# Optimization experiments

Measured on AMD Instinct MI355X. Metric: run time of the kernel, lower is better.

## Reference

```python
import jax, jax.numpy as jnp
import numpy as np

D_MODEL, D_K, D_V = 1024, 64, 64
B, S = 4, 4096


def setup_inputs() -> dict:
    key = jax.random.key(0)
    ks = jax.random.split(key, 13)
    s = 1.0 / np.sqrt(D_MODEL)
    inp = {
        "q": jax.random.normal(ks[0], (B, S, D_MODEL), jnp.float32),
        "k": jax.random.normal(ks[1], (B, S, D_MODEL), jnp.float32),
        "v": jax.random.normal(ks[2], (B, S, D_MODEL), jnp.float32),
        "mask": jax.random.randint(ks[3], (1, S, S), 0, 2, jnp.int32),
        "Wq": jax.random.normal(ks[4], (D_K, D_MODEL), jnp.float32) * s,
        "bq": jax.random.normal(ks[5], (D_K,), jnp.float32) * s,
        "Wk": jax.random.normal(ks[6], (D_K, D_MODEL), jnp.float32) * s,
        "bk": jax.random.normal(ks[7], (D_K,), jnp.float32) * s,
        "Wv": jax.random.normal(ks[8], (D_V, D_MODEL), jnp.float32) * s,
        "bv": jax.random.normal(ks[9], (D_V,), jnp.float32) * s,
        "Wo": jax.random.normal(ks[10], (D_MODEL, D_V), jnp.float32) / np.sqrt(D_V),
        "bo": jax.random.normal(ks[11], (D_MODEL,), jnp.float32) / np.sqrt(D_V),
    }
    return inp


def reference(q, k, v, mask, Wq, bq, Wk, bk, Wv, bv, Wo, bo):
    # linear projections (torch Linear: x @ W.T + b)
    qh = jnp.einsum("bsd,kd->bsk", q, Wq) + bq   # [B,S,d_k]
    kh = jnp.einsum("bsd,kd->bsk", k, Wk) + bk   # [B,S,d_k]
    vh = jnp.einsum("bsd,vd->bsv", v, Wv) + bv   # [B,S,d_v]
    scale = 1.0 / jnp.sqrt(jnp.float32(D_K))
    scores = jnp.einsum("bqk,bmk->bqm", qh, kh) * scale  # [B,S,S]
    scores = jnp.where(mask == 0, jnp.float32(-1e9), scores)
    attn = jax.nn.softmax(scores, axis=-1)
    out = jnp.einsum("bqm,bmv->bqv", attn, vh)   # [B,S,d_v]
    return jnp.einsum("bqv,dv->bqd", out, Wo) + bo
```

## Files before the change

kernel.cpp:

```cpp
#include <hip/hip_runtime.h>
#include <cmath>

typedef __attribute__((ext_vector_type(8))) short bf16x8;
typedef __attribute__((ext_vector_type(4))) short bf16x4;
typedef __attribute__((ext_vector_type(4))) float f32x4;

constexpr int B_ = 4;
constexpr int S_ = 4096;
constexpr int DM_ = 1024;
constexpr int DK_ = 64;
constexpr int NROW = B_ * S_;

__device__ __forceinline__ short f2bf(float x) {
  union { float f; unsigned u; } c; c.f = x;
  unsigned r = (c.u + 0x7FFF + ((c.u >> 16) & 1)) >> 16;
  return (short)r;
}
__device__ __forceinline__ float bf2f(short h) {
  union { float f; unsigned u; } c; c.u = ((unsigned)(unsigned short)h) << 16;
  return c.f;
}

__global__ __launch_bounds__(256) void maskpack(
    const int* __restrict__ mask, unsigned long long* __restrict__ bits) {
  const int wid = (blockIdx.x * 256 + threadIdx.x) >> 6;
  const int lane = threadIdx.x & 63;
  const size_t base = (size_t)wid * 4096;
  for (int it = 0; it < 64; ++it) {
    int m = mask[base + it * 64 + lane];
    unsigned long long b = __ballot(m != 0);
    if (lane == 0) bits[(size_t)wid * 64 + it] = b;
  }
}

__global__ __launch_bounds__(256) void proj_mfma(
    const float* __restrict__ q, const float* __restrict__ k,
    const float* __restrict__ v,
    const float* __restrict__ Wq, const float* __restrict__ bq,
    const float* __restrict__ Wk, const float* __restrict__ bk,
    const float* __restrict__ Wv, const float* __restrict__ bv,
    short* __restrict__ qh, short* __restrict__ kh, short* __restrict__ vhT) {
  const int mat = blockIdx.z;
  const float* X    = mat == 0 ? q  : (mat == 1 ? k  : v);
  const float* W    = mat == 0 ? Wq : (mat == 1 ? Wk : Wv);
  const float* bias = mat == 0 ? bq : (mat == 1 ? bk : bv);

  __shared__ float Xs[128][68];
  __shared__ short Ws[64][72];

  const int t = threadIdx.x;
  const int row0 = blockIdx.x * 128;
  const int lane = t & 63, w = t >> 6, quad = lane >> 4, l16 = lane & 15;

  f32x4 acc[2][4] = {};

  for (int k0 = 0; k0 < DM_; k0 += 64) {
    __syncthreads();
    {
      const int rr = t >> 3, cc = (t & 7) * 8;
#pragma unroll
      for (int pass = 0; pass < 4; ++pass) {
        int r = pass * 32 + rr;
        const float* src = X + (size_t)(row0 + r) * DM_ + k0 + cc;
        *(f32x4*)&Xs[r][cc]     = *(const f32x4*)src;
        *(f32x4*)&Xs[r][cc + 4] = *(const f32x4*)(src + 4);
      }
    }
    {
      int c = t >> 2, kk = (t & 3) * 16;
      const float* src = W + (size_t)c * DM_ + k0 + kk;
      f32x4 a0 = *(const f32x4*)src, a1 = *(const f32x4*)(src + 4);
      f32x4 a2 = *(const f32x4*)(src + 8), a3 = *(const f32x4*)(src + 12);
      bf16x8 w0, w1;
#pragma unroll
      for (int j = 0; j < 4; ++j) {
        w0[j] = f2bf(a0[j]); w0[j + 4] = f2bf(a1[j]);
        w1[j] = f2bf(a2[j]); w1[j + 4] = f2bf(a3[j]);
      }
      *(bf16x8*)&Ws[c][kk]     = w0;
      *(bf16x8*)&Ws[c][kk + 8] = w1;
    }
    __syncthreads();

#pragma unroll
    for (int c = 0; c < 2; ++c) {
      bf16x8 bw[4];
#pragma unroll
      for (int ct = 0; ct < 4; ++ct)
        bw[ct] = *(const bf16x8*)&Ws[16 * ct + l16][c * 32 + quad * 8];
#pragma unroll
      for (int rt = 0; rt < 2; ++rt) {
        const float* xp = &Xs[32 * w + 16 * rt + l16][c * 32 + quad * 8];
        f32x4 x0 = *(const f32x4*)xp;
        f32x4 x1 = *(const f32x4*)(xp + 4);
        bf16x8 ahi, alo;
#pragma unroll
        for (int j = 0; j < 4; ++j) {
          short h0 = f2bf(x0[j]); ahi[j] = h0;     alo[j]     = f2bf(x0[j] - bf2f(h0));
          short h1 = f2bf(x1[j]); ahi[j + 4] = h1; alo[j + 4] = f2bf(x1[j] - bf2f(h1));
        }
#pragma unroll
        for (int ct = 0; ct < 4; ++ct) {
          acc[rt][ct] = __builtin_amdgcn_mfma_f32_16x16x32_bf16(ahi, bw[ct], acc[rt][ct], 0, 0, 0);
          acc[rt][ct] = __builtin_amdgcn_mfma_f32_16x16x32_bf16(alo, bw[ct], acc[rt][ct], 0, 0, 0);
        }
      }
    }
  }

  float bs[4];
#pragma unroll
  for (int ct = 0; ct < 4; ++ct) bs[ct] = bias[16 * ct + l16];

  short* dstq = (mat == 0) ? qh : kh;
#pragma unroll
  for (int rt = 0; rt < 2; ++rt)
#pragma unroll
    for (int ct = 0; ct < 4; ++ct)
#pragma unroll
      for (int reg = 0; reg < 4; ++reg) {
        int r = row0 + 32 * w + 16 * rt + quad * 4 + reg;
        int c = 16 * ct + l16;
        short hv = f2bf(acc[rt][ct][reg] + bs[ct]);
        if (mat == 2)
          vhT[((size_t)(r >> 12) * DK_ + c) * S_ + (r & 4095)] = hv;
        else
          dstq[(size_t)r * DK_ + c] = hv;
      }
}

__global__ __launch_bounds__(256) void attn_mfma(
    const short* __restrict__ qh, const short* __restrict__ kh,
    const short* __restrict__ vhT, const unsigned int* __restrict__ mbits,
    float* __restrict__ Opart, float* __restrict__ mpart,
    float* __restrict__ lpart, int ns) {
  __shared__ short ks[64][72];
  __shared__ short vt[64][72];
  __shared__ short ps[4][16][72];

  const int b = blockIdx.z;
  const int split = blockIdx.y;
  const int q0 = blockIdx.x * 64;
  const int t = threadIdx.x, lane = t & 63, w = t >> 6;
  const int quad = lane >> 4, l16 = lane & 15;
  const int myq = q0 + 16 * w + l16;

  const int kt0 = split * (S_ / ns);
  const int kt1 = kt0 + S_ / ns;

  bf16x8 qf[2];
  {
    const short* src = qh + ((size_t)b * S_ + myq) * DK_ + quad * 8;
    qf[0] = *(const bf16x8*)src;
    qf[1] = *(const bf16x8*)(src + 32);
  }

  f32x4 ao[4] = {};
  float m_i = -INFINITY, l_i = 0.0f;

  const int sr = t >> 2;
  const int sseg = t & 3;

  for (int kt = kt0; kt < kt1; kt += 64) {
    __syncthreads();
    {
      const short* srck = kh + ((size_t)b * S_ + kt + sr) * DK_;
      *(bf16x8*)&ks[sr][8 * sseg]       = *(const bf16x8*)(srck + 8 * sseg);
      *(bf16x8*)&ks[sr][8 * (sseg + 4)] = *(const bf16x8*)(srck + 8 * (sseg + 4));
      const short* srcv = vhT + ((size_t)b * DK_ + sr) * S_ + kt;
      *(bf16x8*)&vt[sr][8 * sseg]       = *(const bf16x8*)(srcv + 8 * sseg);
      *(bf16x8*)&vt[sr][8 * (sseg + 4)] = *(const bf16x8*)(srcv + 8 * (sseg + 4));
    }
    const uint2 mw = *(const uint2*)&mbits[(size_t)myq * 128 + (kt >> 5)];
    __syncthreads();

    f32x4 sacc[4] = {};
#pragma unroll
    for (int c = 0; c < 2; ++c)
#pragma unroll
      for (int tt = 0; tt < 4; ++tt) {
        bf16x8 a = *(const bf16x8*)&ks[16 * tt + l16][c * 32 + quad * 8];
        sacc[tt] = __builtin_amdgcn_mfma_f32_16x16x32_bf16(a, qf[c], sacc[tt], 0, 0, 0);
      }

    float sc[16];
#pragma unroll
    for (int tt = 0; tt < 4; ++tt) {
      unsigned wrd = (tt & 2) ? mw.y : mw.x;
      int base = (tt & 1) * 16 + quad * 4;
#pragma unroll
      for (int r = 0; r < 4; ++r)
        sc[tt * 4 + r] = ((wrd >> (base + r)) & 1) ? sacc[tt][r] * 0.125f : -1e9f;
    }

    float mx = sc[0];
#pragma unroll
    for (int i = 1; i < 16; ++i) mx = fmaxf(mx, sc[i]);
    mx = fmaxf(mx, __shfl_xor(mx, 16));
    mx = fmaxf(mx, __shfl_xor(mx, 32));
    float m_new = fmaxf(m_i, mx);
    float alpha = __expf(m_i - m_new);
    float p[16], sum = 0.0f;
#pragma unroll
    for (int i = 0; i < 16; ++i) { p[i] = __expf(sc[i] - m_new); sum += p[i]; }
    sum += __shfl_xor(sum, 16);
    sum += __shfl_xor(sum, 32);
    l_i = l_i * alpha + sum;
    m_i = m_new;

#pragma unroll
    for (int tt = 0; tt < 4; ++tt) {
      bf16x4 pk;
#pragma unroll
      for (int r = 0; r < 4; ++r) pk[r] = f2bf(p[tt * 4 + r]);
      *(bf16x4*)&ps[w][l16][16 * tt + quad * 4] = pk;
    }

#pragma unroll
    for (int dt = 0; dt < 4; ++dt)
#pragma unroll
      for (int r = 0; r < 4; ++r) ao[dt][r] *= alpha;

#pragma unroll
    for (int c = 0; c < 2; ++c) {
      bf16x8 bp = *(const bf16x8*)&ps[w][l16][c * 32 + quad * 8];
#pragma unroll
      for (int dt = 0; dt < 4; ++dt) {
        bf16x8 av = *(const bf16x8*)&vt[16 * dt + l16][c * 32 + quad * 8];
        ao[dt] = __builtin_amdgcn_mfma_f32_16x16x32_bf16(av, bp, ao[dt], 0, 0, 0);
      }
    }
  }

  const size_t prow = (size_t)split * NROW + (size_t)b * S_ + myq;
#pragma unroll
  for (int dt = 0; dt < 4; ++dt)
    *(f32x4*)&Opart[prow * DK_ + 16 * dt + quad * 4] = ao[dt];
  if (quad == 0) {
    mpart[prow] = m_i;
    lpart[prow] = l_i;
  }
}

__global__ __launch_bounds__(256) void attn_combine(
    const float* __restrict__ Opart, const float* __restrict__ mpart,
    const float* __restrict__ lpart, short* __restrict__ o_bf, int ns) {
  const int t = threadIdx.x;
  const int row = blockIdx.x * 64 + (t >> 2);
  const int c0 = (t & 3) * 16;

  float M = -INFINITY;
  for (int s = 0; s < ns; ++s) M = fmaxf(M, mpart[(size_t)s * NROW + row]);
  float L = 0.0f, wt[4];
  for (int s = 0; s < ns; ++s) {
    wt[s] = __expf(mpart[(size_t)s * NROW + row] - M);
    L += wt[s] * lpart[(size_t)s * NROW + row];
  }
  float acc[16] = {};
  for (int s = 0; s < ns; ++s) {
    const float* src = Opart + ((size_t)s * NROW + row) * DK_ + c0;
#pragma unroll
    for (int j = 0; j < 16; j += 4) {
      f32x4 vv = *(const f32x4*)(src + j);
#pragma unroll
      for (int r = 0; r < 4; ++r) acc[j + r] += wt[s] * vv[r];
    }
  }
  const float inv = 1.0f / L;
  bf16x8 o0, o1;
#pragma unroll
  for (int j = 0; j < 8; ++j) {
    o0[j] = f2bf(acc[j] * inv);
    o1[j] = f2bf(acc[j + 8] * inv);
  }
  *(bf16x8*)&o_bf[(size_t)row * DK_ + c0]     = o0;
  *(bf16x8*)&o_bf[(size_t)row * DK_ + c0 + 8] = o1;
}

__global__ __launch_bounds__(256) void outproj_mfma(
    const short* __restrict__ o_bf, const float* __restrict__ Wo,
    const float* __restrict__ bo, float* __restrict__ out) {
  __shared__ short os[64][72];
  __shared__ short wos[256][72];

  const int t = threadIdx.x, lane = t & 63, w = t >> 6;
  const int quad = lane >> 4, l16 = lane & 15;
  const int s0 = blockIdx.y * 64;
  const int dm0 = blockIdx.x * 256;

  {
    int r = t >> 2, cq = (t & 3) * 16;
    const short* src = o_bf + (size_t)(s0 + r) * DK_ + cq;
    *(bf16x8*)&os[r][cq]     = *(const bf16x8*)src;
    *(bf16x8*)&os[r][cq + 8] = *(const bf16x8*)(src + 8);
  }
#pragma unroll
  for (int pass = 0; pass < 4; ++pass) {
    int r = pass * 64 + (t >> 2), cq = (t & 3) * 16;
    const float* src = Wo + (size_t)(dm0 + r) * DK_ + cq;
    f32x4 a0 = *(const f32x4*)src, a1 = *(const f32x4*)(src + 4);
    f32x4 a2 = *(const f32x4*)(src + 8), a3 = *(const f32x4*)(src + 12);
    bf16x8 v0, v1;
#pragma unroll
    for (int j = 0; j < 4; ++j) {
      v0[j] = f2bf(a0[j]); v0[j + 4] = f2bf(a1[j]);
      v1[j] = f2bf(a2[j]); v1[j + 4] = f2bf(a3[j]);
    }
    *(bf16x8*)&wos[r][cq]     = v0;
    *(bf16x8*)&wos[r][cq + 8] = v1;
  }
  __syncthreads();

  bf16x8 af[2];
#pragma unroll
  for (int c = 0; c < 2; ++c)
    af[c] = *(const bf16x8*)&os[16 * w + l16][c * 32 + quad * 8];

  f32x4 acc[16] = {};
#pragma unroll
  for (int c = 0; c < 2; ++c)
#pragma unroll
    for (int nt = 0; nt < 16; ++nt) {
      bf16x8 bw = *(const bf16x8*)&wos[16 * nt + l16][c * 32 + quad * 8];
      acc[nt] = __builtin_amdgcn_mfma_f32_16x16x32_bf16(af[c], bw, acc[nt], 0, 0, 0);
    }

  float bias_r[16];
#pragma unroll
  for (int nt = 0; nt < 16; ++nt) bias_r[nt] = bo[dm0 + 16 * nt + l16];

#pragma unroll
  for (int nt = 0; nt < 16; ++nt)
#pragma unroll
    for (int reg = 0; reg < 4; ++reg) {
      int s = s0 + 16 * w + quad * 4 + reg;
      int dm = dm0 + 16 * nt + l16;
      out[(size_t)s * DM_ + dm] = acc[nt][reg] + bias_r[nt];
    }
}

extern "C" void kernel_launch(void* const* d_in, const int* in_sizes, int n_in,
                              void* d_out, int out_size, void* d_ws,
                              size_t ws_size, hipStream_t stream) {
  (void)in_sizes; (void)n_in; (void)out_size;
  const float* q  = (const float*)d_in[0];
  const float* k  = (const float*)d_in[1];
  const float* v  = (const float*)d_in[2];
  const int* mask = (const int*)d_in[3];
  const float* Wq = (const float*)d_in[4];
  const float* bq = (const float*)d_in[5];
  const float* Wk = (const float*)d_in[6];
  const float* bk = (const float*)d_in[7];
  const float* Wv = (const float*)d_in[8];
  const float* bv = (const float*)d_in[9];
  const float* Wo = (const float*)d_in[10];
  const float* bo = (const float*)d_in[11];
  float* out = (float*)d_out;

  short* qh  = (short*)d_ws;
  short* kh  = qh + (size_t)NROW * DK_;
  short* vhT = kh + (size_t)NROW * DK_;
  unsigned int* mbits = (unsigned int*)(vhT + (size_t)NROW * DK_);
  short* o_bf = (short*)(mbits + (size_t)S_ * 128);
  float* mpart = (float*)(o_bf + (size_t)NROW * DK_);
  float* lpart = mpart + 4 * NROW;
  float* Opart = lpart + 4 * NROW;

  const size_t base_bytes = (size_t)((char*)Opart - (char*)d_ws);
  const size_t per_split = (size_t)NROW * DK_ * sizeof(float);
  int ns = 1;
  if (ws_size >= base_bytes + 4 * per_split) ns = 4;
  else if (ws_size >= base_bytes + 2 * per_split) ns = 2;

  maskpack<<<1024, 256, 0, stream>>>(mask, (unsigned long long*)mbits);
  proj_mfma<<<dim3(NROW / 128, 1, 3), 256, 0, stream>>>(
      q, k, v, Wq, bq, Wk, bk, Wv, bv, qh, kh, vhT);
  attn_mfma<<<dim3(S_ / 64, ns, B_), 256, 0, stream>>>(
      qh, kh, vhT, mbits, Opart, mpart, lpart, ns);
  attn_combine<<<NROW / 64, 256, 0, stream>>>(Opart, mpart, lpart, o_bf, ns);
  outproj_mfma<<<dim3(DM_ / 256, NROW / 64), 256, 0, stream>>>(o_bf, Wo, bo, out);
}
```

Measured before the change: 390.1 us.

## Double-buffer projection GEMM with async global-to-LDS loads and pre-converted bf16 weights

Folds the weight fp32→bf16 conversion into the mask-packing prep kernel, so the projection kernel reads bf16 weights directly. The projection GEMM now uses direct global_load_lds into XOR-swizzled, double-buffered LDS tiles, overlapping the next tile's load with MFMA compute. Rows per block drop from 128 to 64 to raise block count. The bf16 weights are stored in the Opart workspace region, which later attention kernels overwrite; this is safe only because of stream ordering.

Result: faster. 380.3 us (-2.5%).

```diff
diff --git a/kernel.cpp b/kernel.cpp
--- a/kernel.cpp
+++ b/kernel.cpp
@@ -4,6 +4,9 @@
 typedef __attribute__((ext_vector_type(8))) short bf16x8;
 typedef __attribute__((ext_vector_type(4))) short bf16x4;
 typedef __attribute__((ext_vector_type(4))) float f32x4;
+typedef unsigned int u32;
+typedef __attribute__((address_space(1))) const u32 gu32;
+typedef __attribute__((address_space(3))) u32 lu32;
 
 constexpr int B_ = 4;
 constexpr int S_ = 4096;
@@ -20,92 +23,120 @@
   union { float f; unsigned u; } c; c.u = ((unsigned)(unsigned short)h) << 16;
   return c.f;
 }
-
-__global__ __launch_bounds__(256) void maskpack(
-    const int* __restrict__ mask, unsigned long long* __restrict__ bits) {
-  const int wid = (blockIdx.x * 256 + threadIdx.x) >> 6;
-  const int lane = threadIdx.x & 63;
-  const size_t base = (size_t)wid * 4096;
-  for (int it = 0; it < 64; ++it) {
-    int m = mask[base + it * 64 + lane];
-    unsigned long long b = __ballot(m != 0);
-    if (lane == 0) bits[(size_t)wid * 64 + it] = b;
+__device__ __forceinline__ void gl16(const void* g, void* l) {
+  __builtin_amdgcn_global_load_lds((gu32*)g, (lu32*)l, 16, 0, 0);
+}
+
+__global__ __launch_bounds__(256) void prep(
+    const int* __restrict__ mask, unsigned long long* __restrict__ bits,
+    const float* __restrict__ Wq, const float* __restrict__ Wk,
+    const float* __restrict__ Wv, short* __restrict__ wbf) {
+  if (blockIdx.x < 1024) {
+    const int wid = (blockIdx.x * 256 + threadIdx.x) >> 6;
+    const int lane = threadIdx.x & 63;
+    const size_t base = (size_t)wid * 4096;
+    for (int it = 0; it < 64; ++it) {
+      int m = mask[base + it * 64 + lane];
+      unsigned long long b = __ballot(m != 0);
+      if (lane == 0) bits[(size_t)wid * 64 + it] = b;
+    }
+  } else {
+    const int mat = blockIdx.x - 1024;
+    const float* W = mat == 0 ? Wq : (mat == 1 ? Wk : Wv);
+    short* dst = wbf + (size_t)mat * DK_ * DM_;
+    const int t = threadIdx.x;
+#pragma unroll 4
+    for (int i = 0; i < 32; ++i) {
+      int idx = i * 2048 + t * 8;
+      f32x4 a0 = *(const f32x4*)(W + idx);
+      f32x4 a1 = *(const f32x4*)(W + idx + 4);
+      bf16x8 h;
+#pragma unroll
+      for (int j = 0; j < 4; ++j) { h[j] = f2bf(a0[j]); h[j + 4] = f2bf(a1[j]); }
+      *(bf16x8*)(dst + idx) = h;
+    }
   }
 }
 
 __global__ __launch_bounds__(256) void proj_mfma(
     const float* __restrict__ q, const float* __restrict__ k,
-    const float* __restrict__ v,
-    const float* __restrict__ Wq, const float* __restrict__ bq,
-    const float* __restrict__ Wk, const float* __restrict__ bk,
-    const float* __restrict__ Wv, const float* __restrict__ bv,
+    const float* __restrict__ v, const short* __restrict__ wbf,
+    const float* __restrict__ bq, const float* __restrict__ bk,
+    const float* __restrict__ bv,
     short* __restrict__ qh, short* __restrict__ kh, short* __restrict__ vhT) {
+  __shared__ __align__(16) char smem[49152];
+
   const int mat = blockIdx.z;
-  const float* X    = mat == 0 ? q  : (mat == 1 ? k  : v);
-  const float* W    = mat == 0 ? Wq : (mat == 1 ? Wk : Wv);
+  const char* Xb = (const char*)(mat == 0 ? q : (mat == 1 ? k : v));
+  const char* Wb = (const char*)(wbf + (size_t)mat * DK_ * DM_);
   const float* bias = mat == 0 ? bq : (mat == 1 ? bk : bv);
 
-  __shared__ float Xs[128][68];
-  __shared__ short Ws[64][72];
-
   const int t = threadIdx.x;
-  const int row0 = blockIdx.x * 128;
+  const int row0 = blockIdx.x * 64;
   const int lane = t & 63, w = t >> 6, quad = lane >> 4, l16 = lane & 15;
 
-  f32x4 acc[2][4] = {};
-
-  for (int k0 = 0; k0 < DM_; k0 += 64) {
-    __syncthreads();
-    {
-      const int rr = t >> 3, cc = (t & 7) * 8;
-#pragma unroll
-      for (int pass = 0; pass < 4; ++pass) {
-        int r = pass * 32 + rr;
-        const float* src = X + (size_t)(row0 + r) * DM_ + k0 + cc;
-        *(f32x4*)&Xs[r][cc]     = *(const f32x4*)src;
-        *(f32x4*)&Xs[r][cc + 4] = *(const f32x4*)(src + 4);
-      }
-    }
-    {
-      int c = t >> 2, kk = (t & 3) * 16;
-      const float* src = W + (size_t)c * DM_ + k0 + kk;
-      f32x4 a0 = *(const f32x4*)src, a1 = *(const f32x4*)(src + 4);
-      f32x4 a2 = *(const f32x4*)(src + 8), a3 = *(const f32x4*)(src + 12);
-      bf16x8 w0, w1;
-#pragma unroll
-      for (int j = 0; j < 4; ++j) {
-        w0[j] = f2bf(a0[j]); w0[j + 4] = f2bf(a1[j]);
-        w1[j] = f2bf(a2[j]); w1[j + 4] = f2bf(a3[j]);
-      }
-      *(bf16x8*)&Ws[c][kk]     = w0;
-      *(bf16x8*)&Ws[c][kk + 8] = w1;
-    }
-    __syncthreads();
-
+  f32x4 acc[4] = {};
+
+  auto stage = [&](int buf, int ks) {
+    const int k0 = ks * 64;
+#pragma unroll
+    for (int i = 0; i < 4; ++i) {
+      int o = t * 16 + i * 4096;
+      int row = o >> 8, col = o & 255;
+      int scol = col ^ ((row & 7) << 4);
+      gl16(Xb + (size_t)(row0 + row) * (DM_ * 4) + k0 * 4 + scol,
+           smem + buf * 16384 + o);
+    }
+#pragma unroll
+    for (int i = 0; i < 2; ++i) {
+      int o = t * 16 + i * 4096;
+      int row = o >> 7, col = o & 127;
+      int scol = col ^ ((row & 7) << 4);
+      gl16(Wb + row * 2048 + k0 * 2 + scol,
+           smem + 32768 + buf * 8192 + o);
+    }
+  };
+
+  auto compute = [&](int buf) {
+    const char* xs = smem + buf * 16384;
+    const char* ws = smem + 32768 + buf * 8192;
+    const int xrow = 16 * w + l16;
+    const int xsw = (xrow & 7) << 4;
 #pragma unroll
     for (int c = 0; c < 2; ++c) {
       bf16x8 bw[4];
 #pragma unroll
-      for (int ct = 0; ct < 4; ++ct)
-        bw[ct] = *(const bf16x8*)&Ws[16 * ct + l16][c * 32 + quad * 8];
-#pragma unroll
-      for (int rt = 0; rt < 2; ++rt) {
-        const float* xp = &Xs[32 * w + 16 * rt + l16][c * 32 + quad * 8];
-        f32x4 x0 = *(const f32x4*)xp;
-        f32x4 x1 = *(const f32x4*)(xp + 4);
-        bf16x8 ahi, alo;
-#pragma unroll
-        for (int j = 0; j < 4; ++j) {
-          short h0 = f2bf(x0[j]); ahi[j] = h0;     alo[j]     = f2bf(x0[j] - bf2f(h0));
-          short h1 = f2bf(x1[j]); ahi[j + 4] = h1; alo[j + 4] = f2bf(x1[j] - bf2f(h1));
-        }
-#pragma unroll
-        for (int ct = 0; ct < 4; ++ct) {
-          acc[rt][ct] = __builtin_amdgcn_mfma_f32_16x16x32_bf16(ahi, bw[ct], acc[rt][ct], 0, 0, 0);
-          acc[rt][ct] = __builtin_amdgcn_mfma_f32_16x16x32_bf16(alo, bw[ct], acc[rt][ct], 0, 0, 0);
-        }
+      for (int ct = 0; ct < 4; ++ct) {
+        int wr = 16 * ct + l16;
+        bw[ct] = *(const bf16x8*)(ws + wr * 128 +
+                                  ((c * 64 + quad * 16) ^ ((wr & 7) << 4)));
       }
-    }
+      int xb = xrow * 256 + ((c * 128 + quad * 32) ^ xsw);
+      f32x4 x0 = *(const f32x4*)(xs + xb);
+      f32x4 x1 = *(const f32x4*)(xs + (xb ^ 16));
+      bf16x8 ahi, alo;
+#pragma unroll
+      for (int j = 0; j < 4; ++j) {
+        short h0 = f2bf(x0[j]); ahi[j] = h0;     alo[j]     = f2bf(x0[j] - bf2f(h0));
+        short h1 = f2bf(x1[j]); ahi[j + 4] = h1; alo[j + 4] = f2bf(x1[j] - bf2f(h1));
+      }
+#pragma unroll
+      for (int ct = 0; ct < 4; ++ct) {
+        acc[ct] = __builtin_amdgcn_mfma_f32_16x16x32_bf16(ahi, bw[ct], acc[ct], 0, 0, 0);
+        acc[ct] = __builtin_amdgcn_mfma_f32_16x16x32_bf16(alo, bw[ct], acc[ct], 0, 0, 0);
+      }
+    }
+  };
+
+  stage(0, 0);
+  __syncthreads();
+  int cur = 0;
+#pragma unroll 1
+  for (int ks = 0; ks < 16; ++ks) {
+    if (ks < 15) stage(cur ^ 1, ks + 1);
+    compute(cur);
+    __syncthreads();
+    cur ^= 1;
   }
 
   float bs[4];
@@ -114,19 +145,17 @@
 
   short* dstq = (mat == 0) ? qh : kh;
 #pragma unroll
-  for (int rt = 0; rt < 2; ++rt)
-#pragma unroll
-    for (int ct = 0; ct < 4; ++ct)
-#pragma unroll
-      for (int reg = 0; reg < 4; ++reg) {
-        int r = row0 + 32 * w + 16 * rt + quad * 4 + reg;
-        int c = 16 * ct + l16;
-        short hv = f2bf(acc[rt][ct][reg] + bs[ct]);
-        if (mat == 2)
-          vhT[((size_t)(r >> 12) * DK_ + c) * S_ + (r & 4095)] = hv;
-        else
-          dstq[(size_t)r * DK_ + c] = hv;
-      }
+  for (int ct = 0; ct < 4; ++ct)
+#pragma unroll
+    for (int reg = 0; reg < 4; ++reg) {
+      int r = row0 + 16 * w + quad * 4 + reg;
+      int c = 16 * ct + l16;
+      short hv = f2bf(acc[ct][reg] + bs[ct]);
+      if (mat == 2)
+        vhT[((size_t)(r >> 12) * DK_ + c) * S_ + (r & 4095)] = hv;
+      else
+        dstq[(size_t)r * DK_ + c] = hv;
+    }
 }
 
 __global__ __launch_bounds__(256) void attn_mfma(
@@ -365,6 +394,7 @@
   float* mpart = (float*)(o_bf + (size_t)NROW * DK_);
   float* lpart = mpart + 4 * NROW;
   float* Opart = lpart + 4 * NROW;
+  short* wbf = (short*)Opart;
 
   const size_t base_bytes = (size_t)((char*)Opart - (char*)d_ws);
   const size_t per_split = (size_t)NROW * DK_ * sizeof(float);
@@ -372,9 +402,10 @@
   if (ws_size >= base_bytes + 4 * per_split) ns = 4;
   else if (ws_size >= base_bytes + 2 * per_split) ns = 2;
 
-  maskpack<<<1024, 256, 0, stream>>>(mask, (unsigned long long*)mbits);
-  proj_mfma<<<dim3(NROW / 128, 1, 3), 256, 0, stream>>>(
-      q, k, v, Wq, bq, Wk, bk, Wv, bv, qh, kh, vhT);
+  prep<<<1027, 256, 0, stream>>>(mask, (unsigned long long*)mbits,
+                                 Wq, Wk, Wv, wbf);
+  proj_mfma<<<dim3(NROW / 64, 1, 3), 256, 0, stream>>>(
+      q, k, v, wbf, bq, bk, bv, qh, kh, vhT);
   attn_mfma<<<dim3(S_ / 64, ns, B_), 256, 0, stream>>>(
       qh, kh, vhT, mbits, Opart, mpart, lpart, ns);
   attn_combine<<<NROW / 64, 256, 0, stream>>>(Opart, mpart, lpart, o_bf, ns);
```
